# Kernel tuning notes

Measured on AMD Instinct MI355X. Metric: run time of the kernel, lower is better.

The kernel has to match this reference:

```python
import jax, jax.numpy as jnp
import numpy as np

RADIUS = 0.2
NSAMPLE = 32
USE_XYZ = True


def setup_inputs() -> dict:
    key = jax.random.key(0)
    k1, k2, k3 = jax.random.split(key, 3)
    B, N, NP, C = 16, 4096, 1024, 64
    xyz = jax.random.uniform(k1, (B, N, 3), dtype=jnp.float32)
    new_xyz = jax.random.uniform(k2, (B, NP, 3), dtype=jnp.float32)
    points = jax.random.normal(k3, (B, C, N), dtype=jnp.float32)
    return {"xyz": xyz, "new_xyz": new_xyz, "points": points}


def ball_query(radius, nsample, xyz, new_xyz):
    """Replicates the CUDA ball_query: for each center, the first `nsample`
    points (in index order) with squared distance < radius^2. Unfilled slots
    are set to the first in-radius index (0 if none in radius)."""
    B, N, _ = xyz.shape
    NP = new_xyz.shape[1]
    # [B, NP, N] squared distances
    d2 = jnp.sum((new_xyz[:, :, None, :] - xyz[:, None, :, :]) ** 2, axis=-1)
    mask = d2 < (radius * radius)
    order = jnp.cumsum(mask.astype(jnp.int32), axis=-1)  # 1-based rank among in-radius pts
    cnt = order[..., -1]                                  # [B, NP] in-radius count
    # slot for each point: rank-1 if it is one of the first nsample in-radius, else dummy
    slot = jnp.where(mask & (order <= nsample), order - 1, nsample)
    bb = jnp.arange(B, dtype=jnp.int32)[:, None, None]
    pp = jnp.arange(NP, dtype=jnp.int32)[None, :, None]
    nn = jnp.broadcast_to(jnp.arange(N, dtype=jnp.int32)[None, None, :], (B, NP, N))
    idx = jnp.zeros((B, NP, nsample + 1), dtype=jnp.int32).at[bb, pp, slot].set(nn)
    idx = idx[..., :nsample]
    # replicate first in-radius index into unfilled slots (stays 0 if cnt == 0)
    filled = jnp.arange(nsample)[None, None, :] < jnp.minimum(cnt, nsample)[..., None]
    idx = jnp.where(filled, idx, idx[..., :1])
    return idx


def reference(xyz, new_xyz, points):
    idx = ball_query(RADIUS, NSAMPLE, xyz, new_xyz)          # [B, NP, NS] int32
    # gather xyz: [B, NP, NS, 3] -> [B, 3, NP, NS]
    grouped_xyz = jax.vmap(lambda x, i: x[i])(xyz, idx)
    grouped_xyz = jnp.transpose(grouped_xyz, (0, 3, 1, 2))
    # centroid subtract
    grouped_xyz = grouped_xyz - jnp.transpose(new_xyz, (0, 2, 1))[..., None]
    # gather features: points [B, C, N] -> [B, C, NP, NS]
    grouped_points = jax.vmap(lambda p, i: p[:, i])(points, idx)
    if USE_XYZ:
        new_points = jnp.concatenate([grouped_xyz, grouped_points], axis=1)
    else:
        new_points = grouped_points
    return new_points
```

## Files before the change

### kernel.cpp

```cpp
#include <hip/hip_runtime.h>
#include <hip/hip_bf16.h>

constexpr int B  = 16;
constexpr int N  = 4096;
constexpr int NP = 1024;
constexpr int C  = 64;
constexpr int NS = 32;
constexpr int OC = C + 3;
constexpr float R2 = 0.2f * 0.2f;

typedef float v4f __attribute__((ext_vector_type(4)));
typedef int   v4i __attribute__((ext_vector_type(4)));

__global__ __launch_bounds__(256)
void ball_query_kernel(const float* __restrict__ xyz,
                       const float* __restrict__ new_xyz,
                       float* __restrict__ out,
                       int* __restrict__ ws_idx)
{
    const int wid  = (blockIdx.x << 2) + (threadIdx.x >> 6);
    const int lane = threadIdx.x & 63;
    const int b = wid >> 10;
    const int p = wid & (NP - 1);

    const float qx = new_xyz[wid * 3 + 0];
    const float qy = new_xyz[wid * 3 + 1];
    const float qz = new_xyz[wid * 3 + 2];

    const float* xb = xyz + (size_t)b * N * 3;

    float* out_x = out + (((size_t)b * OC + 0) * NP + p) * NS;
    float* out_y = out + (((size_t)b * OC + 1) * NP + p) * NS;
    float* out_z = out + (((size_t)b * OC + 2) * NP + p) * NS;
    int*   idx_p = ws_idx + (size_t)wid * NS;

    float fdx = xb[0] - qx;
    float fdy = xb[1] - qy;
    float fdz = xb[2] - qz;
    int   fidx = 0;

    int cnt = 0;
    for (int base = 0; base < N && cnt < NS; base += 128) {
        const int j0 = base + lane;
        const int j1 = base + 64 + lane;

        const float x0 = xb[j0 * 3 + 0];
        const float y0 = xb[j0 * 3 + 1];
        const float z0 = xb[j0 * 3 + 2];
        const float x1 = xb[j1 * 3 + 0];
        const float y1 = xb[j1 * 3 + 1];
        const float z1 = xb[j1 * 3 + 2];

        const float dx0 = x0 - qx, dy0 = y0 - qy, dz0 = z0 - qz;
        const float dx1 = x1 - qx, dy1 = y1 - qy, dz1 = z1 - qz;
        const float d20 = __fadd_rn(__fadd_rn(__fmul_rn(dx0, dx0),
                                              __fmul_rn(dy0, dy0)),
                                    __fmul_rn(dz0, dz0));
        const float d21 = __fadd_rn(__fadd_rn(__fmul_rn(dx1, dx1),
                                              __fmul_rn(dy1, dy1)),
                                    __fmul_rn(dz1, dz1));
        const bool in0 = d20 < R2;
        const bool in1 = d21 < R2;
        const unsigned long long m0 = __ballot(in0);
        const unsigned long long m1 = __ballot(in1);

        if (cnt == 0) {
            if (m0 != 0ull) {
                const int fl = __ffsll(m0) - 1;
                fdx = __shfl(dx0, fl, 64);
                fdy = __shfl(dy0, fl, 64);
                fdz = __shfl(dz0, fl, 64);
                fidx = base + fl;
            } else if (m1 != 0ull) {
                const int fl = __ffsll(m1) - 1;
                fdx = __shfl(dx1, fl, 64);
                fdy = __shfl(dy1, fl, 64);
                fdz = __shfl(dz1, fl, 64);
                fidx = base + 64 + fl;
            }
        }

        const unsigned long long below = (1ull << lane) - 1ull;
        if (in0) {
            const int slot = cnt + (int)__popcll(m0 & below);
            if (slot < NS) {
                idx_p[slot] = j0;
                out_x[slot] = dx0;
                out_y[slot] = dy0;
                out_z[slot] = dz0;
            }
        }
        const int c0 = cnt + (int)__popcll(m0);
        if (in1) {
            const int slot = c0 + (int)__popcll(m1 & below);
            if (slot < NS) {
                idx_p[slot] = j1;
                out_x[slot] = dx1;
                out_y[slot] = dy1;
                out_z[slot] = dz1;
            }
        }
        cnt = c0 + (int)__popcll(m1);
    }

    const int cntc = cnt < NS ? cnt : NS;
    if (lane >= cntc && lane < NS) {
        idx_p[lane] = fidx;
        out_x[lane] = fdx;
        out_y[lane] = fdy;
        out_z[lane] = fdz;
    }
}

__global__ __launch_bounds__(256)
void group_points_kernel(const float* __restrict__ points,
                         const int* __restrict__ ws_idx,
                         float* __restrict__ out)
{
    __shared__ float s_row[2 * N];

    const int bc = blockIdx.x;
    const int b  = bc >> 5;
    const int c2 = (bc & 31) * 2;

    const v4f* row4 = (const v4f*)(points + ((size_t)b * C + c2) * N);
    v4f* s4 = (v4f*)s_row;
    #pragma unroll
    for (int i = threadIdx.x; i < 2 * N / 4; i += 256)
        s4[i] = row4[i];
    __syncthreads();

    const v4i* idx4 = (const v4i*)(ws_idx + (size_t)b * NP * NS);
    v4f* out0 = (v4f*)(out + ((size_t)b * OC + 3 + c2) * NP * NS);
    v4f* out1 = (v4f*)(out + ((size_t)b * OC + 4 + c2) * NP * NS);

    for (int t = threadIdx.x; t < NP * NS / 4; t += 256) {
        const v4i id = idx4[t];
        v4f va, vb;
        va.x = s_row[id.x];
        va.y = s_row[id.y];
        va.z = s_row[id.z];
        va.w = s_row[id.w];
        vb.x = s_row[N + id.x];
        vb.y = s_row[N + id.y];
        vb.z = s_row[N + id.z];
        vb.w = s_row[N + id.w];
        __builtin_nontemporal_store(va, &out0[t]);
        __builtin_nontemporal_store(vb, &out1[t]);
    }
}

extern "C" void kernel_launch(void* const* d_in, const int* in_sizes, int n_in,
                              void* d_out, int out_size, void* d_ws, size_t ws_size,
                              hipStream_t stream)
{
    const float* xyz     = (const float*)d_in[0];
    const float* new_xyz = (const float*)d_in[1];
    const float* points  = (const float*)d_in[2];
    float* out = (float*)d_out;
    int* ws_idx = (int*)d_ws;

    ball_query_kernel<<<(B * NP) / 4, 256, 0, stream>>>(xyz, new_xyz, out, ws_idx);

    group_points_kernel<<<B * (C / 2), 256, 0, stream>>>(points, ws_idx, out);
}
```

Baseline: 195.2 us.

## Transpose points to point-major layout and gather feature rows per query

A transpose of points into [B,N,C] now runs as extra blocks fused into the ball-query launch. The gather kernel is restructured so each wave handles one query: it loads 32 contiguous 64-channel rows and transposes them through padded LDS to write the channel-major output. This replaces the old scheme, in which every block staged two full channel rows in LDS and did random LDS lookups across all queries. The cost is an extra write and read of the transposed points buffer, plus smaller, less coalesced output stores, since each wave writes 32-float segments per channel.

New measurement: 196.8 us. About the same (+0.8%).

```diff
diff --git a/kernel.cpp b/kernel.cpp
--- a/kernel.cpp
+++ b/kernel.cpp
@@ -13,12 +13,39 @@
 typedef int   v4i __attribute__((ext_vector_type(4)));
 
 __global__ __launch_bounds__(256)
-void ball_query_kernel(const float* __restrict__ xyz,
-                       const float* __restrict__ new_xyz,
-                       float* __restrict__ out,
-                       int* __restrict__ ws_idx)
+void prep_kernel(const float* __restrict__ xyz,
+                 const float* __restrict__ new_xyz,
+                 const float* __restrict__ points,
+                 float* __restrict__ out,
+                 int* __restrict__ ws_idx,
+                 float* __restrict__ pointsT)
 {
-    const int wid  = (blockIdx.x << 2) + (threadIdx.x >> 6);
+    __shared__ float tile[64][65];
+
+    if (blockIdx.x < 1024) {
+        const int tb  = blockIdx.x;
+        const int b   = tb >> 6;
+        const int n0  = (tb & 63) << 6;
+        const int col = threadIdx.x & 63;
+        const int r0  = (threadIdx.x >> 6) << 4;
+
+        const float* src = points + (size_t)b * C * N + n0;
+        #pragma unroll
+        for (int k = 0; k < 16; ++k) {
+            const int c = r0 + k;
+            tile[c][col] = src[(size_t)c * N + col];
+        }
+        __syncthreads();
+        float* dst = pointsT + (size_t)b * N * C + (size_t)n0 * C;
+        #pragma unroll
+        for (int k = 0; k < 16; ++k) {
+            const int n = r0 + k;
+            dst[(size_t)n * C + col] = tile[col][n];
+        }
+        return;
+    }
+
+    const int wid  = ((blockIdx.x - 1024) << 2) + (threadIdx.x >> 6);
     const int lane = threadIdx.x & 63;
     const int b = wid >> 10;
     const int p = wid & (NP - 1);
@@ -113,40 +140,42 @@
 }
 
 __global__ __launch_bounds__(256)
-void group_points_kernel(const float* __restrict__ points,
-                         const int* __restrict__ ws_idx,
-                         float* __restrict__ out)
+void gather_kernel(const float* __restrict__ pointsT,
+                   const int* __restrict__ ws_idx,
+                   float* __restrict__ out)
 {
-    __shared__ float s_row[2 * N];
+    __shared__ float sbuf[4][NS * 65];
 
-    const int bc = blockIdx.x;
-    const int b  = bc >> 5;
-    const int c2 = (bc & 31) * 2;
+    const int g    = blockIdx.x;
+    const int b    = g & 15;
+    const int wave = threadIdx.x >> 6;
+    const int lane = threadIdx.x & 63;
+    const int p    = ((g >> 4) << 2) + wave;
 
-    const v4f* row4 = (const v4f*)(points + ((size_t)b * C + c2) * N);
-    v4f* s4 = (v4f*)s_row;
+    float* sb = &sbuf[wave][0];
+    const int* idx_p = ws_idx + ((size_t)b * NP + p) * NS;
+    const int myidx = (lane < NS) ? idx_p[lane] : 0;
+
+    const float* rb = pointsT + (size_t)b * N * C;
+
+    float vals[NS];
     #pragma unroll
-    for (int i = threadIdx.x; i < 2 * N / 4; i += 256)
-        s4[i] = row4[i];
-    __syncthreads();
+    for (int s = 0; s < NS; ++s) {
+        const int rn = __shfl(myidx, s, 64);
+        vals[s] = rb[(size_t)rn * C + lane];
+    }
+    #pragma unroll
+    for (int s = 0; s < NS; ++s)
+        sb[s * 65 + lane] = vals[s];
 
-    const v4i* idx4 = (const v4i*)(ws_idx + (size_t)b * NP * NS);
-    v4f* out0 = (v4f*)(out + ((size_t)b * OC + 3 + c2) * NP * NS);
-    v4f* out1 = (v4f*)(out + ((size_t)b * OC + 4 + c2) * NP * NS);
-
-    for (int t = threadIdx.x; t < NP * NS / 4; t += 256) {
-        const v4i id = idx4[t];
-        v4f va, vb;
-        va.x = s_row[id.x];
-        va.y = s_row[id.y];
-        va.z = s_row[id.z];
-        va.w = s_row[id.w];
-        vb.x = s_row[N + id.x];
-        vb.y = s_row[N + id.y];
-        vb.z = s_row[N + id.z];
-        vb.w = s_row[N + id.w];
-        __builtin_nontemporal_store(va, &out0[t]);
-        __builtin_nontemporal_store(vb, &out1[t]);
+    const int s    = lane & 31;
+    const int half = lane >> 5;
+    float* ob = out + ((size_t)b * OC + 3) * NP * NS + (size_t)p * NS;
+    #pragma unroll
+    for (int j = 0; j < 32; ++j) {
+        const int c = 2 * j + half;
+        const float v = sb[s * 65 + c];
+        __builtin_nontemporal_store(v, ob + (size_t)c * NP * NS + s);
     }
 }
 
@@ -158,9 +187,12 @@
     const float* new_xyz = (const float*)d_in[1];
     const float* points  = (const float*)d_in[2];
     float* out = (float*)d_out;
-    int* ws_idx = (int*)d_ws;
 
-    ball_query_kernel<<<(B * NP) / 4, 256, 0, stream>>>(xyz, new_xyz, out, ws_idx);
+    int*   ws_idx  = (int*)d_ws;
+    float* pointsT = (float*)((char*)d_ws + ((size_t)2 << 20));
 
-    group_points_kernel<<<B * (C / 2), 256, 0, stream>>>(points, ws_idx, out);
+    prep_kernel<<<1024 + (B * NP) / 4, 256, 0, stream>>>(
+        xyz, new_xyz, points, out, ws_idx, pointsT);
+
+    gather_kernel<<<(B * NP) / 4, 256, 0, stream>>>(pointsT, ws_idx, out);
 }
```
